# Kernel tuning notes

Measured on AMD Instinct MI355X. Metric: run time of the kernel, lower is better.

The kernel has to match this reference:

```python
import jax, jax.numpy as jnp
import numpy as np

B, H, S, D = 2, 16, 2048, 64

def setup_inputs() -> dict:
    key = jax.random.key(0)
    kq, kk, kv = jax.random.split(key, 3)
    Q = jax.random.normal(kq, (B, H, S, D), dtype=jnp.float32)
    K = jax.random.normal(kk, (B, H, S, D), dtype=jnp.float32)
    V = jax.random.normal(kv, (B, H, S, D), dtype=jnp.float32)
    # causal mask: True means 'masked out' (filled with -inf), as in torch.masked_fill
    mask = jnp.triu(jnp.ones((S, S), dtype=bool), k=1)[None, None, :, :]
    return {"Q": Q, "K": K, "V": V, "mask": mask}

def reference(Q, K, V, mask):
    head_dim = jnp.asarray(K.shape[-1], dtype=Q.dtype)
    # a_scaled = Q @ K^T / sqrt(d)   -> [B,H,S,S]
    scores = jnp.einsum('bhqd,bhkd->bhqk', Q, K) / jnp.sqrt(head_dim)
    scores = jnp.where(mask, -jnp.inf, scores)
    # NOTE: the original custom softmax subtracts the GLOBAL max of the whole
    # tensor (torch.max(x) with no dim), not a per-row max. Reproduce faithfully.
    m = jnp.max(scores)
    e = jnp.exp(scores - m)
    attn = e / jnp.sum(e, axis=-1, keepdims=True)
    return jnp.einsum('bhqk,bhkd->bhqd', attn, V)
```

## Files before the change

### kernel.cpp

```cpp
#include <hip/hip_runtime.h>
#include <hip/hip_bf16.h>
#include <cstdint>
#include <cstddef>

#define SLEN 2048
#define DH   64
#define NHEADS 32
#define LOG2E 1.44269504088896340736f

#define PRE_TILE 16384
#define PRE_HEAD (32 * PRE_TILE)
#define PRE_TOTAL ((size_t)NHEADS * PRE_HEAD)

typedef short  bf16x8 __attribute__((ext_vector_type(8)));
typedef float  f32x4  __attribute__((ext_vector_type(4)));

__device__ __forceinline__ unsigned short f2bf(float f) {
    __hip_bfloat16 h = __float2bfloat16(f);
    return *reinterpret_cast<unsigned short*>(&h);
}
__device__ __forceinline__ unsigned int pk2(float a, float b) {
    return (unsigned int)f2bf(a) | ((unsigned int)f2bf(b) << 16);
}

__global__ __launch_bounds__(256) void prep(const float* __restrict__ Kg,
                                            const float* __restrict__ Vg,
                                            unsigned short* __restrict__ ws)
{
    const int bid = blockIdx.x;
    const int tid = threadIdx.x;
    if (bid < 2048) {
        const int cid  = bid * 256 + tid;
        const int h    = cid >> 14;
        const int rem  = cid & 16383;
        const int jt   = rem >> 9;
        const int rem2 = rem & 511;
        const int kci  = rem2 >> 6;
        const int l    = rem2 & 63;
        const int t = kci >> 1, c = kci & 1, g = l >> 4, m = l & 15;
        const float* src =
            Kg + ((size_t)h * SLEN + 64 * jt + 16 * t + m) * DH + 32 * c + 8 * g;
        float4 a = *reinterpret_cast<const float4*>(src);
        float4 b = *reinterpret_cast<const float4*>(src + 4);
        bf16x8 o;
        o[0]=(short)f2bf(a.x); o[1]=(short)f2bf(a.y);
        o[2]=(short)f2bf(a.z); o[3]=(short)f2bf(a.w);
        o[4]=(short)f2bf(b.x); o[5]=(short)f2bf(b.y);
        o[6]=(short)f2bf(b.z); o[7]=(short)f2bf(b.w);
        *(bf16x8*)((char*)ws + (size_t)h * PRE_HEAD + (size_t)jt * PRE_TILE
                   + kci * 1024 + l * 16) = o;
    } else {
        __shared__ __attribute__((aligned(16))) unsigned short Vt[64 * 64];
        const int vb = bid - 2048;
        const int h  = vb >> 5;
        const int jt = vb & 31;
        const int kp  = tid >> 3;
        const int do8 = tid & 7;
        const float* s0 =
            Vg + ((size_t)h * SLEN + 64 * jt + 2 * kp) * DH + 8 * do8;
        float4 a0 = *reinterpret_cast<const float4*>(s0);
        float4 a1 = *reinterpret_cast<const float4*>(s0 + 4);
        float4 b0 = *reinterpret_cast<const float4*>(s0 + DH);
        float4 b1 = *reinterpret_cast<const float4*>(s0 + DH + 4);
        float av[8] = {a0.x,a0.y,a0.z,a0.w,a1.x,a1.y,a1.z,a1.w};
        float bv[8] = {b0.x,b0.y,b0.z,b0.w,b1.x,b1.y,b1.z,b1.w};
        #pragma unroll
        for (int j = 0; j < 8; ++j) {
            const int d = 8 * do8 + j;
            const unsigned byte =
                (unsigned)(d * 128) + ((((unsigned)(kp >> 2)) ^ (unsigned)(d & 7)) << 4)
                + (unsigned)((kp & 3) * 4);
            *(unsigned*)((char*)Vt + byte) = pk2(av[j], bv[j]);
        }
        __syncthreads();
        char* base = (char*)ws + (size_t)h * PRE_HEAD + (size_t)jt * PRE_TILE + 8192;
        #pragma unroll
        for (int u = 0; u < 2; ++u) {
            const int cc  = 2 * tid + u;
            const int vci = cc >> 6;
            const int l   = cc & 63;
            const int kc = vci >> 2, dt = vci & 3, g = l >> 4, m = l & 15;
            const int d   = 16 * dt + m;
            const int kch = 4 * kc + g;
            bf16x8 v = *(const bf16x8*)((const char*)Vt + d * 128
                        + (((unsigned)kch ^ (unsigned)(d & 7)) << 4));
            *(bf16x8*)(base + vci * 1024 + l * 16) = v;
        }
    }
}

__global__ __launch_bounds__(256, 2) void fattn_r(const float* __restrict__ Qg,
                                                  const unsigned short* __restrict__ KV,
                                                  float* __restrict__ Og)
{
    __shared__ __attribute__((aligned(16))) unsigned short Plds[4][2][16 * 64];

    const int bid   = blockIdx.x;
    const int hi    = bid >> 8;
    const int qtile = (bid & 15) ^ (hi ? 15 : 0);
    const int head  = (bid >> 4) & 31;
    const int Qb    = qtile * 128;

    const float* Qp = Qg + (size_t)head * SLEN * DH;
    const char*  KH = (const char*)KV + (size_t)head * PRE_HEAD;
    float*       Op = Og + (size_t)head * SLEN * DH;

    const int tid  = threadIdx.x;
    const int w    = tid >> 6;
    const int lane = tid & 63;
    const int g    = lane >> 4;
    const int m    = lane & 15;

    char* P0 = (char*)&Plds[w][0][0];
    char* P1 = (char*)&Plds[w][1][0];
    const unsigned pswz = ((unsigned)(m & 7)) << 4;

    bf16x8 qf[2][2];
    {
        const float sc = 0.125f * LOG2E;
        #pragma unroll
        for (int h = 0; h < 2; ++h) {
            const int qrow = Qb + 32 * w + 16 * h + m;
            #pragma unroll
            for (int c = 0; c < 2; ++c) {
                const float* src = Qp + (size_t)qrow * DH + 32 * c + 8 * g;
                float4 a = *reinterpret_cast<const float4*>(src);
                float4 b = *reinterpret_cast<const float4*>(src + 4);
                bf16x8 qv;
                qv[0]=(short)f2bf(a.x*sc); qv[1]=(short)f2bf(a.y*sc);
                qv[2]=(short)f2bf(a.z*sc); qv[3]=(short)f2bf(a.w*sc);
                qv[4]=(short)f2bf(b.x*sc); qv[5]=(short)f2bf(b.y*sc);
                qv[6]=(short)f2bf(b.z*sc); qv[7]=(short)f2bf(b.w*sc);
                qf[h][c] = qv;
            }
        }
    }

    f32x4 o0[4], o1[4];
    #pragma unroll
    for (int dt = 0; dt < 4; ++dt) { o0[dt] = (f32x4){0,0,0,0}; o1[dt] = (f32x4){0,0,0,0}; }
    float mr0 = -1e30f, lr0 = 0.f, mr1 = -1e30f, lr1 = 0.f;

    const int q0 = Qb + 32 * w + m;
    const int q1 = q0 + 16;
    const int nt = 2 * qtile + 1 + (w >> 1);

    const char* tb = KH;
    for (int jt = 0; jt < nt; ++jt, tb += PRE_TILE) {
        const bool last = (jt == nt - 1);
        const int  kvb  = jt * 64;

        bf16x8 kf[8];
        #pragma unroll
        for (int i = 0; i < 8; ++i)
            kf[i] = *(const bf16x8*)(tb + i * 1024 + lane * 16);

        f32x4 s0[4], s1[4];
        #pragma unroll
        for (int t = 0; t < 4; ++t) { s0[t] = (f32x4){0,0,0,0}; s1[t] = (f32x4){0,0,0,0}; }
        #pragma unroll
        for (int c = 0; c < 2; ++c) {
            #pragma unroll
            for (int t = 0; t < 4; ++t)
                s0[t] = __builtin_amdgcn_mfma_f32_16x16x32_bf16(kf[2*t+c], qf[0][c], s0[t], 0, 0, 0);
            #pragma unroll
            for (int t = 0; t < 4; ++t)
                s1[t] = __builtin_amdgcn_mfma_f32_16x16x32_bf16(kf[2*t+c], qf[1][c], s1[t], 0, 0, 0);
        }

        bf16x8 vf[8];
        #pragma unroll
        for (int i = 0; i < 8; ++i)
            vf[i] = *(const bf16x8*)(tb + 8192 + i * 1024 + lane * 16);

        #pragma unroll
        for (int h = 0; h < 2; ++h) {
            f32x4* s   = h ? s1 : s0;
            float& mr  = h ? mr1 : mr0;
            float& lr  = h ? lr1 : lr0;
            f32x4* o   = h ? o1 : o0;
            const int q = h ? q1 : q0;
            char*  Pb  = h ? P1 : P0;

            float mx = -1e30f;
            #pragma unroll
            for (int t = 0; t < 4; ++t) {
                #pragma unroll
                for (int r = 0; r < 4; ++r) {
                    float v = s[t][r];
                    if (last) {
                        const int kk = kvb + 16 * t + 4 * g + r;
                        v = (kk > q) ? -1e30f : v;
                    }
                    s[t][r] = v;
                    mx = fmaxf(mx, v);
                }
            }
            mx = fmaxf(mx, __shfl_xor(mx, 16));
            mx = fmaxf(mx, __shfl_xor(mx, 32));

            if (__any(mx > mr)) {
                const float mnew = fmaxf(mr, mx);
                const float fs   = exp2f(mr - mnew);
                mr = mnew;
                lr *= fs;
                float fso[4];
                #pragma unroll
                for (int r = 0; r < 4; ++r)
                    fso[r] = __shfl(fs, (lane & 48) | (4 * g + r));
                #pragma unroll
                for (int dt = 0; dt < 4; ++dt) {
                    #pragma unroll
                    for (int r = 0; r < 4; ++r) o[dt][r] *= fso[r];
                }
            }

            float ps = 0.f;
            #pragma unroll
            for (int t = 0; t < 4; ++t) {
                const float p0 = exp2f(s[t][0] - mr);
                const float p1 = exp2f(s[t][1] - mr);
                const float p2 = exp2f(s[t][2] - mr);
                const float p3 = exp2f(s[t][3] - mr);
                ps += (p0 + p1) + (p2 + p3);
                uint2 e;
                e.x = pk2(p0, p1);
                e.y = pk2(p2, p3);
                const unsigned byte = (unsigned)(m * 128 + 32 * t + 8 * g);
                *(uint2*)(Pb + (byte ^ pswz)) = e;
            }
            ps += __shfl_xor(ps, 16);
            ps += __shfl_xor(ps, 32);
            lr += ps;
        }

        #pragma unroll
        for (int kc = 0; kc < 2; ++kc) {
            const unsigned ab = ((unsigned)(m * 128 + 64 * kc + 16 * g)) ^ pswz;
            bf16x8 pa0 = *(const bf16x8*)(P0 + ab);
            bf16x8 pa1 = *(const bf16x8*)(P1 + ab);
            #pragma unroll
            for (int dt = 0; dt < 4; ++dt) {
                o0[dt] = __builtin_amdgcn_mfma_f32_16x16x32_bf16(pa0, vf[kc*4+dt], o0[dt], 0, 0, 0);
                o1[dt] = __builtin_amdgcn_mfma_f32_16x16x32_bf16(pa1, vf[kc*4+dt], o1[dt], 0, 0, 0);
            }
        }
    }

    #pragma unroll
    for (int h = 0; h < 2; ++h) {
        const float invl = 1.0f / (h ? lr1 : lr0);
        f32x4* o = h ? o1 : o0;
        float invo[4];
        #pragma unroll
        for (int r = 0; r < 4; ++r)
            invo[r] = __shfl(invl, (lane & 48) | (4 * g + r));
        #pragma unroll
        for (int r = 0; r < 4; ++r) {
            const int qrow = Qb + 32 * w + 16 * h + 4 * g + r;
            float* dst = Op + (size_t)qrow * DH;
            #pragma unroll
            for (int dt = 0; dt < 4; ++dt) dst[16 * dt + m] = o[dt][r] * invo[r];
        }
    }
}

__global__ __launch_bounds__(256, 4) void fattn_s(const float* __restrict__ Qg,
                                                  const float* __restrict__ Kg,
                                                  const float* __restrict__ Vg,
                                                  float* __restrict__ Og)
{
    __shared__ __attribute__((aligned(16))) unsigned short Klds[128 * DH];
    __shared__ __attribute__((aligned(16))) unsigned short Vlds[DH * 128];
    __shared__ __attribute__((aligned(16))) unsigned short Plds[4][16 * 128];

    const int bid = blockIdx.x;
    const int hi4 = bid >> 8;
    const int lo8 = bid & 255;
    const int qx  = (int)((0x0F101F00u >> (8 * hi4)) & 31u);
    const int qt  = (lo8 & 31) ^ qx;
    const int bh  = (hi4 << 3) | (lo8 >> 5);
    const int qb  = qt * 64;

    const float* Qp = Qg + (size_t)bh * SLEN * DH;
    const float* Kp = Kg + (size_t)bh * SLEN * DH;
    const float* Vp = Vg + (size_t)bh * SLEN * DH;
    float*       Op = Og + (size_t)bh * SLEN * DH;

    const int tid  = threadIdx.x;
    const int w    = tid >> 6;
    const int lane = tid & 63;
    const int g    = lane >> 4;
    const int m    = lane & 15;

    bf16x8 qf[2];
    {
        const float sc = 0.125f * LOG2E;
        const int qrow = qb + 16 * w + m;
        #pragma unroll
        for (int c = 0; c < 2; ++c) {
            const float* src = Qp + (size_t)qrow * DH + 32 * c + 8 * g;
            float4 a = *reinterpret_cast<const float4*>(src);
            float4 b = *reinterpret_cast<const float4*>(src + 4);
            bf16x8 qv;
            qv[0]=(short)f2bf(a.x*sc); qv[1]=(short)f2bf(a.y*sc);
            qv[2]=(short)f2bf(a.z*sc); qv[3]=(short)f2bf(a.w*sc);
            qv[4]=(short)f2bf(b.x*sc); qv[5]=(short)f2bf(b.y*sc);
            qv[6]=(short)f2bf(b.z*sc); qv[7]=(short)f2bf(b.w*sc);
            qf[c] = qv;
        }
    }

    f32x4 o[4];
    #pragma unroll
    for (int dt = 0; dt < 4; ++dt) o[dt] = (f32x4){0.f, 0.f, 0.f, 0.f};
    float mrun = -1e30f, lrun = 0.f;

    const int klim = qb + 64;
    const int nt   = (qt + 2) >> 1;

    const int rk = tid & 127, hk = tid >> 7;
    const int kp = tid & 63,  dq = tid >> 6;

    char* Pw = (char*)&Plds[w][0];
    const unsigned pswz = ((unsigned)(m & 7)) << 4;
    const int q = qb + 16 * w + m;

    for (int jt = 0; jt < nt; ++jt) {
        const int kvb    = jt * 128;
        const int kwidth = min(128, klim - kvb);
        const bool last  = (jt == nt - 1);

        if (rk < kwidth) {
            const float4* s4 = reinterpret_cast<const float4*>(
                Kp + (size_t)(kvb + rk) * DH + 32 * hk);
            float4 x[8];
            #pragma unroll
            for (int i = 0; i < 8; ++i) x[i] = s4[i];
            const unsigned rswz = ((unsigned)(rk & 7)) << 4;
            #pragma unroll
            for (int c = 0; c < 4; ++c) {
                bf16x8 kb;
                kb[0]=(short)f2bf(x[2*c].x);   kb[1]=(short)f2bf(x[2*c].y);
                kb[2]=(short)f2bf(x[2*c].z);   kb[3]=(short)f2bf(x[2*c].w);
                kb[4]=(short)f2bf(x[2*c+1].x); kb[5]=(short)f2bf(x[2*c+1].y);
                kb[6]=(short)f2bf(x[2*c+1].z); kb[7]=(short)f2bf(x[2*c+1].w);
                const unsigned byte = (unsigned)(rk * 128 + 64 * hk + 16 * c);
                *(bf16x8*)((char*)Klds + (byte ^ rswz)) = kb;
            }
        }
        if (2 * kp < kwidth) {
            const float* s0 = Vp + (size_t)(kvb + 2 * kp) * DH + 16 * dq;
            float av[16], bv[16];
            #pragma unroll
            for (int i = 0; i < 4; ++i) {
                float4 ta = *reinterpret_cast<const float4*>(s0 + 4 * i);
                float4 tb = *reinterpret_cast<const float4*>(s0 + DH + 4 * i);
                av[4*i]=ta.x; av[4*i+1]=ta.y; av[4*i+2]=ta.z; av[4*i+3]=ta.w;
                bv[4*i]=tb.x; bv[4*i+1]=tb.y; bv[4*i+2]=tb.z; bv[4*i+3]=tb.w;
            }
            #pragma unroll
            for (int j = 0; j < 16; ++j) {
                const int d = 16 * dq + j;
                const unsigned byte = (unsigned)(d * 256 + 4 * kp);
                *(unsigned*)((char*)Vlds + (byte ^ (((unsigned)(d & 7)) << 4))) =
                    pk2(av[j], bv[j]);
            }
        }
        __syncthreads();

        f32x4 s[8];
        #pragma unroll
        for (int t = 0; t < 8; ++t) {
            if (16 * t < kwidth) {
                s[t] = (f32x4){0.f, 0.f, 0.f, 0.f};
                #pragma unroll
                for (int c = 0; c < 2; ++c) {
                    const unsigned row  = (unsigned)(16 * t + m);
                    const unsigned byte =
                        (row * 128u + (unsigned)(32 * c + 8 * g) * 2u) ^ ((row & 7u) << 4);
                    bf16x8 kf = *(const bf16x8*)((const char*)Klds + byte);
                    s[t] = __builtin_amdgcn_mfma_f32_16x16x32_bf16(kf, qf[c], s[t], 0, 0, 0);
                }
            }
        }

        float mx = -1e30f;
        #pragma unroll
        for (int t = 0; t < 8; ++t) {
            if (16 * t < kwidth) {
                #pragma unroll
                for (int r = 0; r < 4; ++r) {
                    float v = s[t][r];
                    if (last) {
                        const int kk = kvb + 16 * t + 4 * g + r;
                        v = (kk > q) ? -1e30f : v;
                    }
                    s[t][r] = v;
                    mx = fmaxf(mx, v);
                }
            }
        }
        mx = fmaxf(mx, __shfl_xor(mx, 16));
        mx = fmaxf(mx, __shfl_xor(mx, 32));
        const float mnew = fmaxf(mrun, mx);
        const float fs   = exp2f(mrun - mnew);
        mrun = mnew;

        float psum = 0.f;
        #pragma unroll
        for (int t = 0; t < 8; ++t) {
            if (16 * t < kwidth) {
                const float p0 = exp2f(s[t][0] - mnew);
                const float p1 = exp2f(s[t][1] - mnew);
                const float p2 = exp2f(s[t][2] - mnew);
                const float p3 = exp2f(s[t][3] - mnew);
                psum += (p0 + p1) + (p2 + p3);
                uint2 e;
                e.x = pk2(p0, p1);
                e.y = pk2(p2, p3);
                const unsigned byte = (unsigned)(m * 256 + 32 * t + 8 * g);
                *(uint2*)(Pw + (byte ^ pswz)) = e;
            }
        }
        psum += __shfl_xor(psum, 16);
        psum += __shfl_xor(psum, 32);
        lrun = lrun * fs + psum;

        float fso[4];
        #pragma unroll
        for (int r = 0; r < 4; ++r)
            fso[r] = __shfl(fs, (lane & 48) | (4 * g + r));
        #pragma unroll
        for (int dt = 0; dt < 4; ++dt) {
            #pragma unroll
            for (int r = 0; r < 4; ++r) o[dt][r] *= fso[r];
        }

        const int kclim = kwidth >> 5;
        #pragma unroll
        for (int kc = 0; kc < 4; ++kc) {
            if (kc < kclim) {
                const unsigned ab = ((unsigned)(m * 256 + 64 * kc + 16 * g)) ^ pswz;
                bf16x8 pa = *(const bf16x8*)(Pw + ab);
                #pragma unroll
                for (int dt = 0; dt < 4; ++dt) {
                    const unsigned d  = (unsigned)(16 * dt + m);
                    const unsigned vby =
                        (d * 256u + (unsigned)(64 * kc + 16 * g)) ^ ((d & 7u) << 4);
                    bf16x8 vfb = *(const bf16x8*)((const char*)Vlds + vby);
                    o[dt] = __builtin_amdgcn_mfma_f32_16x16x32_bf16(pa, vfb, o[dt], 0, 0, 0);
                }
            }
        }
        __syncthreads();
    }

    const float invl = 1.0f / lrun;
    float invo[4];
    #pragma unroll
    for (int r = 0; r < 4; ++r)
        invo[r] = __shfl(invl, (lane & 48) | (4 * g + r));
    #pragma unroll
    for (int r = 0; r < 4; ++r) {
        const int qrow = qb + 16 * w + 4 * g + r;
        float* dst = Op + (size_t)qrow * DH;
        #pragma unroll
        for (int dt = 0; dt < 4; ++dt) dst[16 * dt + m] = o[dt][r] * invo[r];
    }
}

extern "C" void kernel_launch(void* const* d_in, const int* in_sizes, int n_in,
                              void* d_out, int out_size, void* d_ws, size_t ws_size,
                              hipStream_t stream) {
    const float* Q = (const float*)d_in[0];
    const float* K = (const float*)d_in[1];
    const float* V = (const float*)d_in[2];
    float* O = (float*)d_out;
    if (ws_size >= PRE_TOTAL) {
        unsigned short* ws = (unsigned short*)d_ws;
        prep<<<dim3(3072), dim3(256), 0, stream>>>(K, V, ws);
        fattn_r<<<dim3(512), dim3(256), 0, stream>>>(Q, ws, O);
    } else {
        fattn_s<<<dim3(1024), dim3(256), 0, stream>>>(Q, K, V, O);
    }
}
```

Measured before the change: 169.8 us.

## Split attention blocks to 64 query rows with one row-group per wave

Each wave now owns 16 query rows instead of two 16-row groups, blocks cover 64 query rows, and the launch doubles to 1024 blocks with a raised occupancy bound. The aim is more parallelism, finer causal load balancing through the new block-to-tile mapping, and lower register pressure so more waves fit per CU. In exchange, each K/V tile read from the workspace is reused by half as many query rows, so global/L2 traffic for K/V roughly doubles.

```diff
diff --git a/kernel.cpp b/kernel.cpp
--- a/kernel.cpp
+++ b/kernel.cpp
@@ -89,17 +89,19 @@
     }
 }
 
-__global__ __launch_bounds__(256, 2) void fattn_r(const float* __restrict__ Qg,
+__global__ __launch_bounds__(256, 4) void fattn_w(const float* __restrict__ Qg,
                                                   const unsigned short* __restrict__ KV,
                                                   float* __restrict__ Og)
 {
-    __shared__ __attribute__((aligned(16))) unsigned short Plds[4][2][16 * 64];
-
-    const int bid   = blockIdx.x;
-    const int hi    = bid >> 8;
-    const int qtile = (bid & 15) ^ (hi ? 15 : 0);
-    const int head  = (bid >> 4) & 31;
-    const int Qb    = qtile * 128;
+    __shared__ __attribute__((aligned(16))) unsigned short Plds[4][16 * 64];
+
+    const int bid = blockIdx.x;
+    const int hi4 = bid >> 8;
+    const int lo8 = bid & 255;
+    const int qx  = (int)((0x0F101F00u >> (8 * hi4)) & 31u);
+    const int qt  = (lo8 & 31) ^ qx;
+    const int head = (hi4 << 3) | (lo8 >> 5);
+    const int qb  = qt * 64;
 
     const float* Qp = Qg + (size_t)head * SLEN * DH;
     const char*  KH = (const char*)KV + (size_t)head * PRE_HEAD;
@@ -111,39 +113,34 @@
     const int g    = lane >> 4;
     const int m    = lane & 15;
 
-    char* P0 = (char*)&Plds[w][0][0];
-    char* P1 = (char*)&Plds[w][1][0];
+    char* Pw = (char*)&Plds[w][0];
     const unsigned pswz = ((unsigned)(m & 7)) << 4;
 
-    bf16x8 qf[2][2];
+    bf16x8 qf[2];
     {
         const float sc = 0.125f * LOG2E;
-        #pragma unroll
-        for (int h = 0; h < 2; ++h) {
-            const int qrow = Qb + 32 * w + 16 * h + m;
-            #pragma unroll
-            for (int c = 0; c < 2; ++c) {
-                const float* src = Qp + (size_t)qrow * DH + 32 * c + 8 * g;
-                float4 a = *reinterpret_cast<const float4*>(src);
-                float4 b = *reinterpret_cast<const float4*>(src + 4);
-                bf16x8 qv;
-                qv[0]=(short)f2bf(a.x*sc); qv[1]=(short)f2bf(a.y*sc);
-                qv[2]=(short)f2bf(a.z*sc); qv[3]=(short)f2bf(a.w*sc);
-                qv[4]=(short)f2bf(b.x*sc); qv[5]=(short)f2bf(b.y*sc);
-                qv[6]=(short)f2bf(b.z*sc); qv[7]=(short)f2bf(b.w*sc);
-                qf[h][c] = qv;
-            }
-        }
-    }
-
-    f32x4 o0[4], o1[4];
-    #pragma unroll
-    for (int dt = 0; dt < 4; ++dt) { o0[dt] = (f32x4){0,0,0,0}; o1[dt] = (f32x4){0,0,0,0}; }
-    float mr0 = -1e30f, lr0 = 0.f, mr1 = -1e30f, lr1 = 0.f;
-
-    const int q0 = Qb + 32 * w + m;
-    const int q1 = q0 + 16;
-    const int nt = 2 * qtile + 1 + (w >> 1);
+        const int qrow = qb + 16 * w + m;
+        #pragma unroll
+        for (int c = 0; c < 2; ++c) {
+            const float* src = Qp + (size_t)qrow * DH + 32 * c + 8 * g;
+            float4 a = *reinterpret_cast<const float4*>(src);
+            float4 b = *reinterpret_cast<const float4*>(src + 4);
+            bf16x8 qv;
+            qv[0]=(short)f2bf(a.x*sc); qv[1]=(short)f2bf(a.y*sc);
+            qv[2]=(short)f2bf(a.z*sc); qv[3]=(short)f2bf(a.w*sc);
+            qv[4]=(short)f2bf(b.x*sc); qv[5]=(short)f2bf(b.y*sc);
+            qv[6]=(short)f2bf(b.z*sc); qv[7]=(short)f2bf(b.w*sc);
+            qf[c] = qv;
+        }
+    }
+
+    f32x4 o[4];
+    #pragma unroll
+    for (int dt = 0; dt < 4; ++dt) o[dt] = (f32x4){0.f, 0.f, 0.f, 0.f};
+    float mr = -1e30f, lr = 0.f;
+
+    const int q  = qb + 16 * w + m;
+    const int nt = qt + 1;
 
     const char* tb = KH;
     for (int jt = 0; jt < nt; ++jt, tb += PRE_TILE) {
@@ -155,17 +152,14 @@
         for (int i = 0; i < 8; ++i)
             kf[i] = *(const bf16x8*)(tb + i * 1024 + lane * 16);
 
-        f32x4 s0[4], s1[4];
-        #pragma unroll
-        for (int t = 0; t < 4; ++t) { s0[t] = (f32x4){0,0,0,0}; s1[t] = (f32x4){0,0,0,0}; }
+        f32x4 s[4];
+        #pragma unroll
+        for (int t = 0; t < 4; ++t) s[t] = (f32x4){0.f, 0.f, 0.f, 0.f};
         #pragma unroll
         for (int c = 0; c < 2; ++c) {
             #pragma unroll
             for (int t = 0; t < 4; ++t)
-                s0[t] = __builtin_amdgcn_mfma_f32_16x16x32_bf16(kf[2*t+c], qf[0][c], s0[t], 0, 0, 0);
-            #pragma unroll
-            for (int t = 0; t < 4; ++t)
-                s1[t] = __builtin_amdgcn_mfma_f32_16x16x32_bf16(kf[2*t+c], qf[1][c], s1[t], 0, 0, 0);
+                s[t] = __builtin_amdgcn_mfma_f32_16x16x32_bf16(kf[2*t+c], qf[c], s[t], 0, 0, 0);
         }
 
         bf16x8 vf[8];
@@ -173,95 +167,78 @@
         for (int i = 0; i < 8; ++i)
             vf[i] = *(const bf16x8*)(tb + 8192 + i * 1024 + lane * 16);
 
-        #pragma unroll
-        for (int h = 0; h < 2; ++h) {
-            f32x4* s   = h ? s1 : s0;
-            float& mr  = h ? mr1 : mr0;
-            float& lr  = h ? lr1 : lr0;
-            f32x4* o   = h ? o1 : o0;
-            const int q = h ? q1 : q0;
-            char*  Pb  = h ? P1 : P0;
-
-            float mx = -1e30f;
-            #pragma unroll
-            for (int t = 0; t < 4; ++t) {
+        float mx = -1e30f;
+        #pragma unroll
+        for (int t = 0; t < 4; ++t) {
+            #pragma unroll
+            for (int r = 0; r < 4; ++r) {
+                float v = s[t][r];
+                if (last) {
+                    const int kk = kvb + 16 * t + 4 * g + r;
+                    v = (kk > q) ? -1e30f : v;
+                }
+                s[t][r] = v;
+                mx = fmaxf(mx, v);
+            }
+        }
+        mx = fmaxf(mx, __shfl_xor(mx, 16));
+        mx = fmaxf(mx, __shfl_xor(mx, 32));
+
+        if (__any(mx > mr)) {
+            const float mnew = fmaxf(mr, mx);
+            const float fs   = exp2f(mr - mnew);
+            mr = mnew;
+            lr *= fs;
+            float fso[4];
+            #pragma unroll
+            for (int r = 0; r < 4; ++r)
+                fso[r] = __shfl(fs, (lane & 48) | (4 * g + r));
+            #pragma unroll
+            for (int dt = 0; dt < 4; ++dt) {
                 #pragma unroll
-                for (int r = 0; r < 4; ++r) {
-                    float v = s[t][r];
-                    if (last) {
-                        const int kk = kvb + 16 * t + 4 * g + r;
-                        v = (kk > q) ? -1e30f : v;
-                    }
-                    s[t][r] = v;
-                    mx = fmaxf(mx, v);
-                }
-            }
-            mx = fmaxf(mx, __shfl_xor(mx, 16));
-            mx = fmaxf(mx, __shfl_xor(mx, 32));
-
-            if (__any(mx > mr)) {
-                const float mnew = fmaxf(mr, mx);
-                const float fs   = exp2f(mr - mnew);
-                mr = mnew;
-                lr *= fs;
-                float fso[4];
-                #pragma unroll
-                for (int r = 0; r < 4; ++r)
-                    fso[r] = __shfl(fs, (lane & 48) | (4 * g + r));
-                #pragma unroll
-                for (int dt = 0; dt < 4; ++dt) {
-                    #pragma unroll
-                    for (int r = 0; r < 4; ++r) o[dt][r] *= fso[r];
-                }
-            }
-
-            float ps = 0.f;
-            #pragma unroll
-            for (int t = 0; t < 4; ++t) {
-                const float p0 = exp2f(s[t][0] - mr);
-                const float p1 = exp2f(s[t][1] - mr);
-                const float p2 = exp2f(s[t][2] - mr);
-                const float p3 = exp2f(s[t][3] - mr);
-                ps += (p0 + p1) + (p2 + p3);
-                uint2 e;
-                e.x = pk2(p0, p1);
-                e.y = pk2(p2, p3);
-                const unsigned byte = (unsigned)(m * 128 + 32 * t + 8 * g);
-                *(uint2*)(Pb + (byte ^ pswz)) = e;
-            }
-            ps += __shfl_xor(ps, 16);
-            ps += __shfl_xor(ps, 32);
-            lr += ps;
-        }
+                for (int r = 0; r < 4; ++r) o[dt][r] *= fso[r];
+            }
+        }
+
+        float ps = 0.f;
+        #pragma unroll
+        for (int t = 0; t < 4; ++t) {
+            const float p0 = exp2f(s[t][0] - mr);
+            const float p1 = exp2f(s[t][1] - mr);
+            const float p2 = exp2f(s[t][2] - mr);
+            const float p3 = exp2f(s[t][3] - mr);
+            ps += (p0 + p1) + (p2 + p3);
+            uint2 e;
+            e.x = pk2(p0, p1);
+            e.y = pk2(p2, p3);
+            const unsigned byte = (unsigned)(m * 128 + 32 * t + 8 * g);
+            *(uint2*)(Pw + (byte ^ pswz)) = e;
+        }
+        ps += __shfl_xor(ps, 16);
+        ps += __shfl_xor(ps, 32);
+        lr += ps;
 
         #pragma unroll
         for (int kc = 0; kc < 2; ++kc) {
             const unsigned ab = ((unsigned)(m * 128 + 64 * kc + 16 * g)) ^ pswz;
-            bf16x8 pa0 = *(const bf16x8*)(P0 + ab);
-            bf16x8 pa1 = *(const bf16x8*)(P1 + ab);
-            #pragma unroll
-            for (int dt = 0; dt < 4; ++dt) {
-                o0[dt] = __builtin_amdgcn_mfma_f32_16x16x32_bf16(pa0, vf[kc*4+dt], o0[dt], 0, 0, 0);
-                o1[dt] = __builtin_amdgcn_mfma_f32_16x16x32_bf16(pa1, vf[kc*4+dt], o1[dt], 0, 0, 0);
-            }
-        }
-    }
-
-    #pragma unroll
-    for (int h = 0; h < 2; ++h) {
-        const float invl = 1.0f / (h ? lr1 : lr0);
-        f32x4* o = h ? o1 : o0;
-        float invo[4];
-        #pragma unroll
-        for (int r = 0; r < 4; ++r)
-            invo[r] = __shfl(invl, (lane & 48) | (4 * g + r));
-        #pragma unroll
-        for (int r = 0; r < 4; ++r) {
-            const int qrow = Qb + 32 * w + 16 * h + 4 * g + r;
-            float* dst = Op + (size_t)qrow * DH;
-            #pragma unroll
-            for (int dt = 0; dt < 4; ++dt) dst[16 * dt + m] = o[dt][r] * invo[r];
-        }
+            bf16x8 pa = *(const bf16x8*)(Pw + ab);
+            #pragma unroll
+            for (int dt = 0; dt < 4; ++dt)
+                o[dt] = __builtin_amdgcn_mfma_f32_16x16x32_bf16(pa, vf[kc*4+dt], o[dt], 0, 0, 0);
+        }
+    }
+
+    const float invl = 1.0f / lr;
+    float invo[4];
+    #pragma unroll
+    for (int r = 0; r < 4; ++r)
+        invo[r] = __shfl(invl, (lane & 48) | (4 * g + r));
+    #pragma unroll
+    for (int r = 0; r < 4; ++r) {
+        const int qrow = qb + 16 * w + 4 * g + r;
+        float* dst = Op + (size_t)qrow * DH;
+        #pragma unroll
+        for (int dt = 0; dt < 4; ++dt) dst[16 * dt + m] = o[dt][r] * invo[r];
     }
 }
 
@@ -480,7 +457,7 @@
     if (ws_size >= PRE_TOTAL) {
         unsigned short* ws = (unsigned short*)d_ws;
         prep<<<dim3(3072), dim3(256), 0, stream>>>(K, V, ws);
-        fattn_r<<<dim3(512), dim3(256), 0, stream>>>(Q, ws, O);
+        fattn_w<<<dim3(1024), dim3(256), 0, stream>>>(Q, ws, O);
     } else {
         fattn_s<<<dim3(1024), dim3(256), 0, stream>>>(Q, K, V, O);
     }
```

Measured after the change: 150.8 us. 11.2% less time.
